# Kernel tuning notes

Hardware: AMD Instinct MI355X
Metric: run time of the kernel (lower is better)

## Reference

```python
import jax, jax.numpy as jnp
import numpy as np

N_NODES = 100000
N_EDGES = 3200000
N_GRAPHS = 125  # 800 nodes per graph
D_IN, D_H1, D_H2, D_OUT = 64, 64, 64, 64


def setup_inputs() -> dict:
    key = jax.random.key(0)
    ks = jax.random.split(key, 9)
    x = jax.random.normal(ks[0], (N_NODES, D_IN), dtype=jnp.float32)
    edge_index = jax.random.randint(ks[1], (2, N_EDGES), 0, N_NODES, dtype=jnp.int32)
    ptr = jnp.arange(0, N_NODES + 1, N_NODES // N_GRAPHS, dtype=jnp.int32)  # [126]
    s1 = 1.0 / np.sqrt(D_IN)
    s2 = 1.0 / np.sqrt(D_H1)
    s3 = 1.0 / np.sqrt(D_H2)
    W1 = jax.random.normal(ks[2], (D_IN, D_H1), jnp.float32) * s1
    b1 = jnp.zeros((D_H1,), jnp.float32)
    W2 = jax.random.normal(ks[3], (D_H1, D_H2), jnp.float32) * s2
    b2 = jnp.zeros((D_H2,), jnp.float32)
    Wf = jax.random.normal(ks[4], (D_H2, D_OUT), jnp.float32) * s3
    bf = jax.random.normal(ks[5], (D_OUT,), jnp.float32) * s3
    return {"x": x, "edge_index": edge_index, "ptr": ptr,
            "W1": W1, "b1": b1, "W2": W2, "b2": b2, "Wf": Wf, "bf": bf}


def _gcn_conv(x, src, dst, deg_inv_sqrt, W, b):
    # PyG GCNConv: h = x @ W; symmetric norm with self-loops; scatter-add; + bias
    h = x @ W                                    # [N, d_out]
    norm = deg_inv_sqrt[src] * deg_inv_sqrt[dst]  # [E]
    msg = h[src] * norm[:, None]                 # [E, d_out] gather + scale
    agg = jax.ops.segment_sum(msg, dst, num_segments=N_NODES)
    # self-loop contribution: norm_ii = deg_inv_sqrt[i]^2
    agg = agg + h * (deg_inv_sqrt ** 2)[:, None]
    return agg + b


def reference(x, edge_index, ptr, W1, b1, W2, b2, Wf, bf):
    src = edge_index[0]
    dst = edge_index[1]
    # degree at target, including the self-loop
    deg = jax.ops.segment_sum(jnp.ones((N_EDGES,), x.dtype), dst,
                              num_segments=N_NODES) + 1.0
    deg_inv_sqrt = jax.lax.rsqrt(deg)

    h = jax.nn.relu(_gcn_conv(x, src, dst, deg_inv_sqrt, W1, b1))
    h = jax.nn.relu(_gcn_conv(h, src, dst, deg_inv_sqrt, W2, b2))
    h = h @ Wf + bf                              # [N, D_OUT]

    # mean aggregation per graph defined by ptr boundaries
    seg = jnp.searchsorted(ptr, jnp.arange(N_NODES, dtype=ptr.dtype),
                           side='right') - 1     # [N] graph id per node
    sums = jax.ops.segment_sum(h, seg, num_segments=N_GRAPHS)  # [G, D_OUT]
    counts = (ptr[1:] - ptr[:-1]).astype(h.dtype)              # [G]
    return sums / counts[:, None]
```

## Files before the change

kernel.cpp:

```cpp
#include <hip/hip_runtime.h>
#include <hip/hip_bf16.h>

#define N_NODES 100000
#define N_EDGES 3200000
#define N_GRAPHS 125
#define D 64
#define NB 800
#define BW 125
#define CAP 5120
#define SC_WGS 512
#define SC_EPW 6250
#define SC_THREADS 1024
#define BUILD_THREADS 512

typedef __bf16 bf16x8 __attribute__((ext_vector_type(8)));
typedef float f32x4 __attribute__((ext_vector_type(4)));
typedef float f32x2 __attribute__((ext_vector_type(2)));

__device__ __forceinline__ float bf_lo(unsigned u) { return __uint_as_float(u << 16); }
__device__ __forceinline__ float bf_hi(unsigned u) { return __uint_as_float(u & 0xffff0000u); }
__device__ __forceinline__ f32x2 bf2(unsigned u) {
    f32x2 r;
    r.x = __uint_as_float(u << 16);
    r.y = __uint_as_float(u & 0xffff0000u);
    return r;
}
__device__ __forceinline__ unsigned short f2bf(float f) {
    unsigned u = __float_as_uint(f);
    return (unsigned short)((u + 0x7fffu + ((u >> 16) & 1u)) >> 16);
}


__global__ void bucket_scatter(const int* __restrict__ src, const int* __restrict__ dst,
                               int* __restrict__ bcursor, unsigned* __restrict__ pairs) {
    __shared__ int bins[NB];
    int wg = blockIdx.x, t = threadIdx.x;
    int e0 = wg * SC_EPW;
    if (t < NB) bins[t] = 0;
    __syncthreads();
    unsigned pw[7];
    int      bl[7];
#pragma unroll
    for (int j = 0; j < 7; ++j) {
        int o = t + j * SC_THREADS;
        if (o < SC_EPW) {
            int i = e0 + o;
            int s = src[i], d = dst[i];
            int b = d / BW;
            pw[j] = ((unsigned)s << 7) | (unsigned)(d - b * BW);
            bl[j] = b;
            atomicAdd(&bins[b], 1);
        }
    }
    __syncthreads();
    if (t < NB) {
        int c = bins[t];
        bins[t] = t * CAP + (c ? atomicAdd(&bcursor[t], c) : 0);
    }
    __syncthreads();
#pragma unroll
    for (int j = 0; j < 7; ++j) {
        int o = t + j * SC_THREADS;
        if (o < SC_EPW) {
            int pos = atomicAdd(&bins[bl[j]], 1);
            pairs[pos] = pw[j];
        }
    }
}

__global__ void bucket_build(const unsigned* __restrict__ pairs, const int* __restrict__ bcursor,
                             int* __restrict__ deg, float* __restrict__ dis,
                             int* __restrict__ row_start, int* __restrict__ csr) {
    __shared__ int h[BW];
    __shared__ int sc[128];
    __shared__ int cur[BW];
    int b = blockIdx.x, t = threadIdx.x;
    int nb = b * BW;
    if (t < BW) h[t] = 0;
    __syncthreads();
    int base = b * CAP, n = bcursor[b];
    for (int i = t; i < n; i += BUILD_THREADS)
        atomicAdd(&h[pairs[base + i] & 127u], 1);
    __syncthreads();
    int own = 0, own_pad = 0;
    if (t < 128) {
        own = (t < BW) ? h[t] : 0;
        own_pad = (own + 7) & ~7;
        sc[t] = own_pad;
    }
    if (t < BW) {
        deg[nb + t] = own;
        dis[nb + t] = rsqrtf((float)own + 1.0f);
    }
    __syncthreads();
    for (int off = 1; off < 128; off <<= 1) {
        int v = (t >= off && t < 128) ? sc[t - off] : 0;
        __syncthreads();
        if (t < 128) sc[t] += v;
        __syncthreads();
    }
    if (t < BW) {
        int rs = base + sc[t] - own_pad;
        row_start[nb + t] = rs;
        cur[t] = rs;
        for (int k = own; k < own_pad; ++k)
            csr[rs + k] = N_NODES;
    }
    __syncthreads();
    for (int i = t; i < n; i += BUILD_THREADS) {
        unsigned p = pairs[base + i];
        int pos = atomicAdd(&cur[p & 127u], 1);
        csr[pos] = (int)(p >> 7);
    }
}


__global__ void mfma_gemm(const unsigned short* __restrict__ Xb, const float* __restrict__ W,
                          const float* __restrict__ dis, unsigned short* __restrict__ Y) {
    int lane = threadIdx.x & 63;
    int wid  = (blockIdx.x * blockDim.x + threadIdx.x) >> 6;
    int nwav = (gridDim.x * blockDim.x) >> 6;
    int nl = lane & 15;
    int kq = lane >> 4;
    int kb = kq * 8;
    union BV { unsigned short s[8]; bf16x8 v; } b0[4], b1[4];
#pragma unroll
    for (int nt = 0; nt < 4; ++nt) {
        int nn = nt * 16 + nl;
#pragma unroll
        for (int j = 0; j < 8; ++j) {
            b0[nt].s[j] = f2bf(W[(kb + j) * 64 + nn]);
            b1[nt].s[j] = f2bf(W[(32 + kb + j) * 64 + nn]);
        }
    }
    const uint4* X4 = (const uint4*)Xb;
    for (int t = wid; t < N_NODES / 16; t += nwav) {
        int m0 = t * 16;
        uint4 a0u = X4[(size_t)(m0 + nl) * 8 + kq];
        uint4 a1u = X4[(size_t)(m0 + nl) * 8 + 4 + kq];
        bf16x8 a0 = __builtin_bit_cast(bf16x8, a0u);
        bf16x8 a1 = __builtin_bit_cast(bf16x8, a1u);
        f32x4 acc[4];
#pragma unroll
        for (int nt = 0; nt < 4; ++nt) {
            acc[nt] = (f32x4){0.0f, 0.0f, 0.0f, 0.0f};
            acc[nt] = __builtin_amdgcn_mfma_f32_16x16x32_bf16(a0, b0[nt].v, acc[nt], 0, 0, 0);
            acc[nt] = __builtin_amdgcn_mfma_f32_16x16x32_bf16(a1, b1[nt].v, acc[nt], 0, 0, 0);
        }
        int rbase = m0 + kq * 4;
        float d0 = dis[rbase], d1 = dis[rbase + 1], d2 = dis[rbase + 2], d3 = dis[rbase + 3];
#pragma unroll
        for (int nt = 0; nt < 4; ++nt) {
            int nn = nt * 16 + nl;
            Y[(size_t)(rbase + 0) * 64 + nn] = f2bf(acc[nt][0] * d0);
            Y[(size_t)(rbase + 1) * 64 + nn] = f2bf(acc[nt][1] * d1);
            Y[(size_t)(rbase + 2) * 64 + nn] = f2bf(acc[nt][2] * d2);
            Y[(size_t)(rbase + 3) * 64 + nn] = f2bf(acc[nt][3] * d3);
        }
    }
}

__global__ void mfma_gemm_f32(const float* __restrict__ X, const float* __restrict__ W,
                              const float* __restrict__ dis, unsigned short* __restrict__ Y) {
    int lane = threadIdx.x & 63;
    int wid  = (blockIdx.x * blockDim.x + threadIdx.x) >> 6;
    int nwav = (gridDim.x * blockDim.x) >> 6;
    int nl = lane & 15;
    int kq = lane >> 4;
    int kb = kq * 8;
    union BV { unsigned short s[8]; bf16x8 v; } b0[4], b1[4];
#pragma unroll
    for (int nt = 0; nt < 4; ++nt) {
        int nn = nt * 16 + nl;
#pragma unroll
        for (int j = 0; j < 8; ++j) {
            b0[nt].s[j] = f2bf(W[(kb + j) * 64 + nn]);
            b1[nt].s[j] = f2bf(W[(32 + kb + j) * 64 + nn]);
        }
    }
    const float4* Xf = (const float4*)X;
    for (int t = wid; t < N_NODES / 16; t += nwav) {
        int m0 = t * 16;
        size_t rb = (size_t)(m0 + nl) * 16;
        float4 f0 = Xf[rb + 2 * kq];
        float4 f1 = Xf[rb + 2 * kq + 1];
        float4 f2 = Xf[rb + 8 + 2 * kq];
        float4 f3 = Xf[rb + 8 + 2 * kq + 1];
        union BV av0, av1;
        av0.s[0] = f2bf(f0.x); av0.s[1] = f2bf(f0.y); av0.s[2] = f2bf(f0.z); av0.s[3] = f2bf(f0.w);
        av0.s[4] = f2bf(f1.x); av0.s[5] = f2bf(f1.y); av0.s[6] = f2bf(f1.z); av0.s[7] = f2bf(f1.w);
        av1.s[0] = f2bf(f2.x); av1.s[1] = f2bf(f2.y); av1.s[2] = f2bf(f2.z); av1.s[3] = f2bf(f2.w);
        av1.s[4] = f2bf(f3.x); av1.s[5] = f2bf(f3.y); av1.s[6] = f2bf(f3.z); av1.s[7] = f2bf(f3.w);
        f32x4 acc[4];
#pragma unroll
        for (int nt = 0; nt < 4; ++nt) {
            acc[nt] = (f32x4){0.0f, 0.0f, 0.0f, 0.0f};
            acc[nt] = __builtin_amdgcn_mfma_f32_16x16x32_bf16(av0.v, b0[nt].v, acc[nt], 0, 0, 0);
            acc[nt] = __builtin_amdgcn_mfma_f32_16x16x32_bf16(av1.v, b1[nt].v, acc[nt], 0, 0, 0);
        }
        int rbase = m0 + kq * 4;
        float d0 = dis[rbase], d1 = dis[rbase + 1], d2 = dis[rbase + 2], d3 = dis[rbase + 3];
#pragma unroll
        for (int nt = 0; nt < 4; ++nt) {
            int nn = nt * 16 + nl;
            Y[(size_t)(rbase + 0) * 64 + nn] = f2bf(acc[nt][0] * d0);
            Y[(size_t)(rbase + 1) * 64 + nn] = f2bf(acc[nt][1] * d1);
            Y[(size_t)(rbase + 2) * 64 + nn] = f2bf(acc[nt][2] * d2);
            Y[(size_t)(rbase + 3) * 64 + nn] = f2bf(acc[nt][3] * d3);
        }
    }
}

__global__ void gather_kernel(const unsigned short* __restrict__ Hb, const int* __restrict__ csr,
                              const int* __restrict__ row_start, const int* __restrict__ deg,
                              const float* __restrict__ dis,
                              const float* __restrict__ bias, void* __restrict__ Out,
                              int do_relu, int fuse_pool, float* __restrict__ P) {
    __shared__ float tmp[4][64];
    int v    = (blockIdx.x * blockDim.x + threadIdx.x) >> 6;
    int lane = threadIdx.x & 63;
    int oct  = lane >> 3;
    int l8   = lane & 7;
    int base = row_start[v];
    int n = deg[v];
    float disv = dis[v];
    const uint4* H4 = (const uint4*)Hb;

    f32x2 c0 = {0.f, 0.f}, c1 = {0.f, 0.f}, c2 = {0.f, 0.f}, c3 = {0.f, 0.f};
    if (oct == 0) {
        uint4 hv = H4[((unsigned)v << 3) + (unsigned)l8];
        c0 = bf2(hv.x); c1 = bf2(hv.y); c2 = bf2(hv.z); c3 = bf2(hv.w);
    }

    int groups = (n + 7) >> 3;
    for (int c = 0; c < groups; c += 8) {
        int sl = csr[base + (c << 3) + lane];
        int gm = min(8, groups - c);
#pragma unroll 4
        for (int t = 0; t < gm; ++t) {
            int ssrc = __shfl(sl, 8 * t + oct);
            uint4 hv = H4[((unsigned)ssrc << 3) + (unsigned)l8];
            c0 += bf2(hv.x); c1 += bf2(hv.y);
            c2 += bf2(hv.z); c3 += bf2(hv.w);
        }
    }
    float a0 = c0.x, a1 = c0.y, a2 = c1.x, a3 = c1.y;
    float a4 = c2.x, a5 = c2.y, a6 = c3.x, a7 = c3.y;
#pragma unroll
    for (int off = 8; off <= 32; off <<= 1) {
        a0 += __shfl_xor(a0, off); a1 += __shfl_xor(a1, off);
        a2 += __shfl_xor(a2, off); a3 += __shfl_xor(a3, off);
        a4 += __shfl_xor(a4, off); a5 += __shfl_xor(a5, off);
        a6 += __shfl_xor(a6, off); a7 += __shfl_xor(a7, off);
    }
    if (oct == 0) {
        float4 blo = ((const float4*)bias)[2 * l8];
        float4 bhi = ((const float4*)bias)[2 * l8 + 1];
        a0 = fmaf(a0, disv, blo.x); a1 = fmaf(a1, disv, blo.y);
        a2 = fmaf(a2, disv, blo.z); a3 = fmaf(a3, disv, blo.w);
        a4 = fmaf(a4, disv, bhi.x); a5 = fmaf(a5, disv, bhi.y);
        a6 = fmaf(a6, disv, bhi.z); a7 = fmaf(a7, disv, bhi.w);
        if (do_relu) {
            a0 = fmaxf(a0, 0.0f); a1 = fmaxf(a1, 0.0f); a2 = fmaxf(a2, 0.0f); a3 = fmaxf(a3, 0.0f);
            a4 = fmaxf(a4, 0.0f); a5 = fmaxf(a5, 0.0f); a6 = fmaxf(a6, 0.0f); a7 = fmaxf(a7, 0.0f);
        }
        if (!fuse_pool) {
            union { unsigned short s[8]; uint4 u; } p;
            p.s[0] = f2bf(a0); p.s[1] = f2bf(a1); p.s[2] = f2bf(a2); p.s[3] = f2bf(a3);
            p.s[4] = f2bf(a4); p.s[5] = f2bf(a5); p.s[6] = f2bf(a6); p.s[7] = f2bf(a7);
            ((uint4*)Out)[((unsigned)v << 3) + (unsigned)l8] = p.u;
        } else {
            float* tr = &tmp[threadIdx.x >> 6][l8 * 8];
            tr[0] = a0; tr[1] = a1; tr[2] = a2; tr[3] = a3;
            tr[4] = a4; tr[5] = a5; tr[6] = a6; tr[7] = a7;
        }
    }
    if (fuse_pool) {
        __syncthreads();
        if (threadIdx.x < 64) {
            int cc = threadIdx.x;
            float s = tmp[0][cc] + tmp[1][cc] + tmp[2][cc] + tmp[3][cc];
            int g = blockIdx.x / 200;
            atomicAdd(&P[g * 64 + cc], s);
        }
    }
}

__global__ void gemm_kernel(const float* __restrict__ X, const float* __restrict__ W,
                            const float* __restrict__ bias, float* __restrict__ Y,
                            int nrows) {
    __shared__ float Ws[64][64];
    for (int i = threadIdx.x; i < 64 * 64; i += 256)
        Ws[i >> 6][i & 63] = W[i];
    __syncthreads();
    int c  = threadIdx.x & 63;
    int rl = threadIdx.x >> 6;
    int r  = blockIdx.x * 4 + rl;
    if (r < nrows) {
        const float* xr = X + (size_t)r * D;
        float dot = 0.0f;
#pragma unroll
        for (int k = 0; k < 64; ++k)
            dot = fmaf(xr[k], Ws[k][c], dot);
        Y[(size_t)r * D + c] = fmaf(dot, 1.0f / 800.0f, bias[c]);
    }
}

extern "C" void kernel_launch(void* const* d_in, const int* in_sizes, int n_in,
                              void* d_out, int out_size, void* d_ws, size_t ws_size,
                              hipStream_t stream) {
    const float* x   = (const float*)d_in[0];
    const int*   ei  = (const int*)d_in[1];
    const int*   src = ei;
    const int*   dst = ei + N_EDGES;
    const float* W1  = (const float*)d_in[3];
    const float* b1  = (const float*)d_in[4];
    const float* W2  = (const float*)d_in[5];
    const float* b2  = (const float*)d_in[6];
    const float* Wf  = (const float*)d_in[7];
    const float* bfp = (const float*)d_in[8];
    float* out = (float*)d_out;

    int*   deg       = (int*)d_ws;
    int*   row_start = deg + 100352;
    int*   bcursor   = row_start + 100352;
    float* P         = (float*)(bcursor + 1024);
    float* dis       = P + 8192;
    int*   csr       = (int*)(dis + 100352);
    float* R         = (float*)(csr + 4096000);
    unsigned short* Ab = (unsigned short*)R;
    unsigned short* Hb = (unsigned short*)(R + 3200064);
    unsigned* pairs  = (unsigned*)(R + 6400128);

    hipMemsetAsync(bcursor, 0, NB * sizeof(int), stream);
    hipMemsetAsync(P, 0, N_GRAPHS * D * sizeof(float), stream);
    hipMemsetAsync(Ab + (size_t)N_NODES * D, 0, D * sizeof(unsigned short), stream);
    bucket_scatter<<<SC_WGS, SC_THREADS, 0, stream>>>(src, dst, bcursor, pairs);
    bucket_build<<<NB, BUILD_THREADS, 0, stream>>>(pairs, bcursor, deg, dis, row_start, csr);

    const int grid4 = (N_NODES + 3) / 4;

    mfma_gemm_f32<<<782, 256, 0, stream>>>(x, W1, dis, Ab);
    gather_kernel<<<grid4, 256, 0, stream>>>(Ab, csr, row_start, deg, dis, b1, Hb, 1, 0, nullptr);

    mfma_gemm<<<782, 256, 0, stream>>>(Hb, W2, dis, Ab);
    gather_kernel<<<grid4, 256, 0, stream>>>(Ab, csr, row_start, deg, dis, b2, nullptr, 1, 1, P);

    gemm_kernel<<<(N_GRAPHS + 3) / 4, 256, 0, stream>>>(P, Wf, bfp, out, N_GRAPHS);
}
```

Measured before the change: 299.5 us.

## Replace bucketed CSR build with global-atomic degree count and direct fill

Replaces the two-pass bucket scatter and per-bucket LDS build with three kernels: a global-atomic degree count, a per-bucket prefix scan that sets row starts and cursors, and a direct CSR fill using global atomics on per-node cursors. This removes the intermediate pairs buffer and its extra write and read pass, but relies on heavily contended global atomics and scattered 4-byte writes. The gather kernel also drops the shuffle-based index broadcast and reads each source index directly from the CSR per octet. The bucket capacity is raised to give more room for padded rows.

After: 636.1 us. 112% more time.

```diff
diff --git a/kernel.cpp b/kernel.cpp
--- a/kernel.cpp
+++ b/kernel.cpp
@@ -7,11 +7,8 @@
 #define D 64
 #define NB 800
 #define BW 125
-#define CAP 5120
-#define SC_WGS 512
-#define SC_EPW 6250
-#define SC_THREADS 1024
-#define BUILD_THREADS 512
+#define CAP 5760
+#define FILL_BLOCKS 3125
 
 typedef __bf16 bf16x8 __attribute__((ext_vector_type(8)));
 typedef float f32x4 __attribute__((ext_vector_type(4)));
@@ -31,87 +28,54 @@
 }
 
 
-__global__ void bucket_scatter(const int* __restrict__ src, const int* __restrict__ dst,
-                               int* __restrict__ bcursor, unsigned* __restrict__ pairs) {
-    __shared__ int bins[NB];
-    int wg = blockIdx.x, t = threadIdx.x;
-    int e0 = wg * SC_EPW;
-    if (t < NB) bins[t] = 0;
-    __syncthreads();
-    unsigned pw[7];
-    int      bl[7];
-#pragma unroll
-    for (int j = 0; j < 7; ++j) {
-        int o = t + j * SC_THREADS;
-        if (o < SC_EPW) {
-            int i = e0 + o;
-            int s = src[i], d = dst[i];
-            int b = d / BW;
-            pw[j] = ((unsigned)s << 7) | (unsigned)(d - b * BW);
-            bl[j] = b;
-            atomicAdd(&bins[b], 1);
-        }
-    }
-    __syncthreads();
-    if (t < NB) {
-        int c = bins[t];
-        bins[t] = t * CAP + (c ? atomicAdd(&bcursor[t], c) : 0);
-    }
-    __syncthreads();
-#pragma unroll
-    for (int j = 0; j < 7; ++j) {
-        int o = t + j * SC_THREADS;
-        if (o < SC_EPW) {
-            int pos = atomicAdd(&bins[bl[j]], 1);
-            pairs[pos] = pw[j];
-        }
-    }
-}
-
-__global__ void bucket_build(const unsigned* __restrict__ pairs, const int* __restrict__ bcursor,
-                             int* __restrict__ deg, float* __restrict__ dis,
-                             int* __restrict__ row_start, int* __restrict__ csr) {
-    __shared__ int h[BW];
+__global__ void deg_count(const int* __restrict__ dst, int* __restrict__ deg) {
+    int i = blockIdx.x * blockDim.x + threadIdx.x;
+    int4 d = ((const int4*)dst)[i];
+    atomicAdd(&deg[d.x], 1);
+    atomicAdd(&deg[d.y], 1);
+    atomicAdd(&deg[d.z], 1);
+    atomicAdd(&deg[d.w], 1);
+}
+
+__global__ void row_build(const int* __restrict__ deg, float* __restrict__ dis,
+                          int* __restrict__ row_start, int* __restrict__ cursor,
+                          int* __restrict__ csr) {
     __shared__ int sc[128];
-    __shared__ int cur[BW];
     int b = blockIdx.x, t = threadIdx.x;
     int nb = b * BW;
-    if (t < BW) h[t] = 0;
-    __syncthreads();
-    int base = b * CAP, n = bcursor[b];
-    for (int i = t; i < n; i += BUILD_THREADS)
-        atomicAdd(&h[pairs[base + i] & 127u], 1);
-    __syncthreads();
     int own = 0, own_pad = 0;
-    if (t < 128) {
-        own = (t < BW) ? h[t] : 0;
+    if (t < BW) {
+        own = deg[nb + t];
         own_pad = (own + 7) & ~7;
-        sc[t] = own_pad;
-    }
-    if (t < BW) {
-        deg[nb + t] = own;
         dis[nb + t] = rsqrtf((float)own + 1.0f);
     }
+    sc[t] = own_pad;
     __syncthreads();
     for (int off = 1; off < 128; off <<= 1) {
-        int v = (t >= off && t < 128) ? sc[t - off] : 0;
+        int v = (t >= off) ? sc[t - off] : 0;
         __syncthreads();
-        if (t < 128) sc[t] += v;
+        sc[t] += v;
         __syncthreads();
     }
     if (t < BW) {
-        int rs = base + sc[t] - own_pad;
+        int rs = b * CAP + sc[t] - own_pad;
         row_start[nb + t] = rs;
-        cur[t] = rs;
+        cursor[nb + t] = rs;
         for (int k = own; k < own_pad; ++k)
             csr[rs + k] = N_NODES;
     }
-    __syncthreads();
-    for (int i = t; i < n; i += BUILD_THREADS) {
-        unsigned p = pairs[base + i];
-        int pos = atomicAdd(&cur[p & 127u], 1);
-        csr[pos] = (int)(p >> 7);
-    }
+}
+
+__global__ void csr_fill(const int* __restrict__ src, const int* __restrict__ dst,
+                         int* __restrict__ cursor, int* __restrict__ csr) {
+    int i = blockIdx.x * blockDim.x + threadIdx.x;
+    int4 s = ((const int4*)src)[i];
+    int4 d = ((const int4*)dst)[i];
+    int p0 = atomicAdd(&cursor[d.x], 1);
+    int p1 = atomicAdd(&cursor[d.y], 1);
+    int p2 = atomicAdd(&cursor[d.z], 1);
+    int p3 = atomicAdd(&cursor[d.w], 1);
+    csr[p0] = s.x; csr[p1] = s.y; csr[p2] = s.z; csr[p3] = s.w;
 }
 
 
@@ -233,16 +197,13 @@
     }
 
     int groups = (n + 7) >> 3;
-    for (int c = 0; c < groups; c += 8) {
-        int sl = csr[base + (c << 3) + lane];
-        int gm = min(8, groups - c);
+    const int* cp = csr + base + oct;
 #pragma unroll 4
-        for (int t = 0; t < gm; ++t) {
-            int ssrc = __shfl(sl, 8 * t + oct);
-            uint4 hv = H4[((unsigned)ssrc << 3) + (unsigned)l8];
-            c0 += bf2(hv.x); c1 += bf2(hv.y);
-            c2 += bf2(hv.z); c3 += bf2(hv.w);
-        }
+    for (int g = 0; g < groups; ++g) {
+        int ssrc = cp[g << 3];
+        uint4 hv = H4[((unsigned)ssrc << 3) + (unsigned)l8];
+        c0 += bf2(hv.x); c1 += bf2(hv.y);
+        c2 += bf2(hv.z); c3 += bf2(hv.w);
     }
     float a0 = c0.x, a1 = c0.y, a2 = c1.x, a3 = c1.y;
     float a4 = c2.x, a5 = c2.y, a6 = c3.x, a7 = c3.y;
@@ -323,20 +284,19 @@
 
     int*   deg       = (int*)d_ws;
     int*   row_start = deg + 100352;
-    int*   bcursor   = row_start + 100352;
-    float* P         = (float*)(bcursor + 1024);
+    int*   cursor    = row_start + 100352;
+    float* P         = (float*)(cursor + 100352);
     float* dis       = P + 8192;
     int*   csr       = (int*)(dis + 100352);
-    float* R         = (float*)(csr + 4096000);
-    unsigned short* Ab = (unsigned short*)R;
-    unsigned short* Hb = (unsigned short*)(R + 3200064);
-    unsigned* pairs  = (unsigned*)(R + 6400128);
-
-    hipMemsetAsync(bcursor, 0, NB * sizeof(int), stream);
+    unsigned short* Ab = (unsigned short*)(csr + 4608000);
+    unsigned short* Hb = Ab + 6400128;
+
+    hipMemsetAsync(deg, 0, 100352 * sizeof(int), stream);
     hipMemsetAsync(P, 0, N_GRAPHS * D * sizeof(float), stream);
     hipMemsetAsync(Ab + (size_t)N_NODES * D, 0, D * sizeof(unsigned short), stream);
-    bucket_scatter<<<SC_WGS, SC_THREADS, 0, stream>>>(src, dst, bcursor, pairs);
-    bucket_build<<<NB, BUILD_THREADS, 0, stream>>>(pairs, bcursor, deg, dis, row_start, csr);
+    deg_count<<<FILL_BLOCKS, 256, 0, stream>>>(dst, deg);
+    row_build<<<NB, 128, 0, stream>>>(deg, dis, row_start, cursor, csr);
+    csr_fill<<<FILL_BLOCKS, 256, 0, stream>>>(src, dst, cursor, csr);
 
     const int grid4 = (N_NODES + 3) / 4;
 
```
